# Kernel optimization log

Hardware: AMD Instinct MI355X
Metric: run time of the kernel (lower is better)

Reference implementation:

```python
import jax, jax.numpy as jnp
import numpy as np

H = 8      # num_attention_heads
DH = 96    # attention_head_size
LN_EPS = 1e-5


def setup_inputs() -> dict:
    key = jax.random.key(0)
    ks = jax.random.split(key, 12)
    B, S, D = 2, 768, 768
    sc = 0.02
    return {
        "hidden_states": jax.random.normal(ks[0], (B, S, D), jnp.float32),
        "distance_matrix": jax.random.uniform(ks[1], (B, S, S), jnp.float32) * 20.0,
        "angle_matrix": jax.random.uniform(ks[2], (B, S, S), jnp.float32) * np.pi,
        "attention_mask": jnp.ones((B, S), jnp.float32),
        "Wq": jax.random.normal(ks[3], (D, D), jnp.float32) * sc,
        "bq": jnp.zeros((D,), jnp.float32),
        "Wk": jax.random.normal(ks[4], (D, D), jnp.float32) * sc,
        "bk": jnp.zeros((D,), jnp.float32),
        "Wv": jax.random.normal(ks[5], (D, D), jnp.float32) * sc,
        "bv": jnp.zeros((D,), jnp.float32),
        "Wd": jax.random.normal(ks[6], (DH,), jnp.float32) * sc,
        "bd": jnp.zeros((DH,), jnp.float32),
        "Wa": jax.random.normal(ks[7], (DH,), jnp.float32) * sc,
        "ba": jnp.zeros((DH,), jnp.float32),
        "Wo": jax.random.normal(ks[8], (D, D), jnp.float32) * sc,
        "bo": jnp.zeros((D,), jnp.float32),
        "ln_g": jnp.ones((D,), jnp.float32),
        "ln_b": jnp.zeros((D,), jnp.float32),
    }


def _heads(x, B, S):
    # [B,S,D] -> [B,H,S,DH]
    return x.reshape(B, S, H, DH).transpose(0, 2, 1, 3)


def reference(hidden_states, distance_matrix, angle_matrix, attention_mask,
              Wq, bq, Wk, bk, Wv, bv, Wd, bd, Wa, ba, Wo, bo, ln_g, ln_b):
    B, S, D = hidden_states.shape
    q = _heads(hidden_states @ Wq.T + bq, B, S)   # [B,H,S,DH]
    k = _heads(hidden_states @ Wk.T + bk, B, S)
    v = _heads(hidden_states @ Wv.T + bv, B, S)

    scores = jnp.einsum('bhid,bhjd->bhij', q, k) / jnp.sqrt(jnp.float32(DH))

    # distance / angle relative-position biases: emb[b,i,j,:] = dist[b,i,j]*Wd + bd
    dist_emb = distance_matrix[..., None] * Wd + bd   # [B,S,S,DH]
    scores = scores + jnp.einsum('bhid,bijd->bhij', q, dist_emb)
    ang_emb = angle_matrix[..., None] * Wa + ba       # [B,S,S,DH]
    scores = scores + jnp.einsum('bhid,bijd->bhij', q, ang_emb)

    # key mask, broadcast over heads and query positions
    scores = scores + (1.0 - attention_mask)[:, None, None, :] * -10000.0

    probs = jax.nn.softmax(scores, axis=-1)           # [B,H,S,S]
    ctx = jnp.einsum('bhij,bhjd->bhid', probs, v)
    ctx = ctx.transpose(0, 2, 1, 3).reshape(B, S, D)  # [B,S,D]

    out = ctx @ Wo.T + bo
    x = out + hidden_states
    mu = jnp.mean(x, axis=-1, keepdims=True)
    var = jnp.var(x, axis=-1, keepdims=True)
    out = (x - mu) * jax.lax.rsqrt(var + LN_EPS) * ln_g + ln_b
    return out, probs
```

## Files before the change

kernel.cpp:

```cpp
#include <hip/hip_runtime.h>
#include <stdint.h>

#define B_  2
#define S_  768
#define D_  768
#define H_  8
#define DH_ 96

typedef unsigned short ushort_t;
typedef __bf16 bf16x8 __attribute__((ext_vector_type(8)));
typedef float  f32x4  __attribute__((ext_vector_type(4)));

__device__ inline ushort_t f2bf(float f) {
    union { float f; unsigned int u; } v; v.f = f;
    unsigned int u = v.u;
    unsigned int r = u + 0x7fffu + ((u >> 16) & 1u);
    return (ushort_t)(r >> 16);
}
__device__ inline float bf2f(ushort_t u) {
    union { unsigned int i; float f; } c; c.i = ((unsigned int)u) << 16;
    return c.f;
}

__device__ inline void glds16(const void* gp, void* lp) {
    auto g = reinterpret_cast<const __attribute__((address_space(1))) uint32_t*>(
        reinterpret_cast<uintptr_t>(gp));
    auto l = reinterpret_cast<__attribute__((address_space(3))) uint32_t*>(
        reinterpret_cast<uintptr_t>(lp));
    __builtin_amdgcn_global_load_lds(g, l, 16, 0, 0);
}

__global__ __launch_bounds__(256) void k_convert(
        const float* __restrict__ X, const float* __restrict__ Wq,
        const float* __restrict__ Wk, const float* __restrict__ Wv,
        const float* __restrict__ Wo,
        ushort_t* __restrict__ Xb, ushort_t* __restrict__ Wb) {
    const int NX4 = (B_ * S_ * D_) / 4;
    const int NW4 = (D_ * D_) / 4;
    int i = blockIdx.x * blockDim.x + threadIdx.x;
    float4 v;
    ushort_t* dst;
    if (i < NX4) {
        v = ((const float4*)X)[i];
        dst = Xb + i * 4;
    } else {
        int wi = i - NX4;
        int sel = wi / NW4;
        int off = wi - sel * NW4;
        const float* src = (sel == 0) ? Wq : (sel == 1) ? Wk : (sel == 2) ? Wv : Wo;
        v = ((const float4*)src)[off];
        dst = Wb + wi * 4;
    }
    ushort4 o;
    o.x = f2bf(v.x); o.y = f2bf(v.y); o.z = f2bf(v.z); o.w = f2bf(v.w);
    *(ushort4*)dst = o;
}

__device__ inline void gemm64_glds(
        const ushort_t* __restrict__ A, int lda,
        const ushort_t* __restrict__ Bt, int ldb,
        int K, int m0, int n0,
        ushort_t* As, ushort_t* Bs, f32x4 acc[2][2]) {
    const int tid  = threadIdx.x;
    const int lane = tid & 63, wave = tid >> 6;
    const int wm = (wave >> 1) * 32, wn = (wave & 1) * 32;
    const int fr = lane & 15, fk = (lane >> 4) * 8;
    const int sr = wave * 16 + (lane >> 2);
    const int sc = (lane & 3) * 8;
    const ushort_t* Ap = A  + (size_t)(m0 + sr) * lda + sc;
    const ushort_t* Bp = Bt + (size_t)(n0 + sr) * ldb + sc;
    ushort_t* AsW = As + wave * 512;
    ushort_t* BsW = Bs + wave * 512;
    for (int kt = 0; kt < K; kt += 32) {
        if (kt) __syncthreads();
        glds16(Ap + kt, AsW);
        glds16(Bp + kt, BsW);
        __syncthreads();
        bf16x8 a0 = *(const bf16x8*)&As[(wm      + fr) * 32 + fk];
        bf16x8 a1 = *(const bf16x8*)&As[(wm + 16 + fr) * 32 + fk];
        bf16x8 b0 = *(const bf16x8*)&Bs[(wn      + fr) * 32 + fk];
        bf16x8 b1 = *(const bf16x8*)&Bs[(wn + 16 + fr) * 32 + fk];
        acc[0][0] = __builtin_amdgcn_mfma_f32_16x16x32_bf16(a0, b0, acc[0][0], 0, 0, 0);
        acc[0][1] = __builtin_amdgcn_mfma_f32_16x16x32_bf16(a0, b1, acc[0][1], 0, 0, 0);
        acc[1][0] = __builtin_amdgcn_mfma_f32_16x16x32_bf16(a1, b0, acc[1][0], 0, 0, 0);
        acc[1][1] = __builtin_amdgcn_mfma_f32_16x16x32_bf16(a1, b1, acc[1][1], 0, 0, 0);
    }
}

__global__ __launch_bounds__(256) void k_qkv(
        const ushort_t* __restrict__ Xb, const ushort_t* __restrict__ Wb,
        const float* __restrict__ bq, const float* __restrict__ bk,
        const float* __restrict__ bv,
        ushort_t* __restrict__ Qb, ushort_t* __restrict__ Kb,
        ushort_t* __restrict__ Vtb) {
    __shared__ __align__(16) ushort_t As[64 * 32];
    __shared__ __align__(16) ushort_t Bs[64 * 32];
    f32x4 acc[2][2];
    #pragma unroll
    for (int i = 0; i < 2; i++)
        #pragma unroll
        for (int j = 0; j < 2; j++) acc[i][j] = (f32x4){0.f, 0.f, 0.f, 0.f};
    const int m0 = blockIdx.y * 64, n0 = blockIdx.x * 64;
    gemm64_glds(Xb, D_, Wb, D_, D_, m0, n0, As, Bs, acc);
    const int lane = threadIdx.x & 63, wave = threadIdx.x >> 6;
    const int wm = (wave >> 1) * 32, wn = (wave & 1) * 32;
    #pragma unroll
    for (int ni = 0; ni < 2; ni++) {
        int gcol = n0 + wn + ni * 16 + (lane & 15);
        int g = gcol / D_, d768 = gcol - g * D_;
        int h = d768 / DH_, d = d768 - h * DH_;
        float bias = (g == 0 ? bq : (g == 1 ? bk : bv))[d768];
        #pragma unroll
        for (int mi = 0; mi < 2; mi++) {
            #pragma unroll
            for (int r = 0; r < 4; r++) {
                int grow = m0 + wm + mi * 16 + (lane >> 4) * 4 + r;
                int b = grow / S_, s = grow - b * S_;
                ushort_t ob = f2bf(acc[mi][ni][r] + bias);
                int bh = b * H_ + h;
                if (g == 0)      Qb[((size_t)bh * S_ + s) * DH_ + d] = ob;
                else if (g == 1) Kb[((size_t)bh * S_ + s) * DH_ + d] = ob;
                else             Vtb[((size_t)bh * DH_ + d) * S_ + s] = ob;
            }
        }
    }
}

__global__ __launch_bounds__(256) void k_qcoef(
        const ushort_t* __restrict__ Qb,
        const float* __restrict__ Wd, const float* __restrict__ bd,
        const float* __restrict__ Wa, const float* __restrict__ ba,
        float* __restrict__ qcoef) {
    const int wave = threadIdx.x >> 6, lane = threadIdx.x & 63;
    const int row = blockIdx.x * 4 + wave;
    const ushort_t* q = Qb + (size_t)row * DH_;
    float e0 = bf2f(q[lane]);
    float c0 = e0 * Wd[lane];
    float c1 = e0 * Wa[lane];
    float c2 = e0 * (bd[lane] + ba[lane]);
    if (lane < 32) {
        int d = 64 + lane;
        float e1 = bf2f(q[d]);
        c0 += e1 * Wd[d];
        c1 += e1 * Wa[d];
        c2 += e1 * (bd[d] + ba[d]);
    }
    #pragma unroll
    for (int o = 32; o > 0; o >>= 1) {
        c0 += __shfl_down(c0, o);
        c1 += __shfl_down(c1, o);
        c2 += __shfl_down(c2, o);
    }
    if (lane == 0) {
        qcoef[row * 3 + 0] = c0;
        qcoef[row * 3 + 1] = c1;
        qcoef[row * 3 + 2] = c2;
    }
}

#define L1B 29696
__global__ __launch_bounds__(256) void k_flash(
        const ushort_t* __restrict__ Qb, const ushort_t* __restrict__ Kb,
        const ushort_t* __restrict__ Vtb, const float* __restrict__ qcoef,
        const float* __restrict__ distm, const float* __restrict__ angm,
        const float* __restrict__ mask,
        float* __restrict__ probs, ushort_t* __restrict__ Ctxb) {
    __shared__ __align__(16) char sm[2 * L1B + 640];
    float* mstat = (float*)(sm + 2 * L1B);
    float* lstat = (float*)(sm + 2 * L1B + 256);
    float* linv  = (float*)(sm + 2 * L1B + 512);
    const int idx = blockIdx.x;
    const int h = idx / 48, rem = idx - h * 48;
    const int b = rem / 24, r0 = (rem - b * 24) * 32;
    const int bh = b * H_ + h;
    const int tid = threadIdx.x, lane = tid & 63, w = tid >> 6;
    const int frn = lane & 15, fko = (lane >> 4) * 8, frg4 = (lane >> 4) * 4;
    const int rg = w & 1, cp = w >> 1;
    const ushort_t* Qbh = Qb + (size_t)bh * S_ * DH_;
    const ushort_t* Kbh = Kb + (size_t)bh * S_ * DH_;
    const ushort_t* Vbh = Vtb + (size_t)bh * DH_ * S_;

    bf16x8 aq[3];
    {
        const ushort_t* qp = Qbh + (size_t)(r0 + rg * 16 + frn) * DH_ + fko;
        aq[0] = *(const bf16x8*)qp;
        aq[1] = *(const bf16x8*)(qp + 32);
        aq[2] = *(const bf16x8*)(qp + 64);
    }
    float qc0[4], qc1[4], qc2[4];
    #pragma unroll
    for (int r = 0; r < 4; r++) {
        const float* qp = qcoef + ((size_t)bh * S_ + r0 + rg * 16 + frg4 + r) * 3;
        qc0[r] = qp[0]; qc1[r] = qp[1]; qc2[r] = qp[2];
    }
    const float isq = 0.10206207261596577f;

    f32x4 acc[24];
    #pragma unroll
    for (int c = 0; c < 12; ++c) {
        char* bufc = sm + (c & 1) * L1B;
        ushort_t* Ks = (ushort_t*)bufc;
        float* Dd = (float*)(bufc + 12288);
        float* Da = (float*)(bufc + 20992);
        #pragma unroll
        for (int k = 0; k < 3; ++k) {
            int i = tid + 256 * k;
            int row = i / 12, cc = (i - row * 12) * 8;
            *(uint4*)(Ks + row * 96 + cc) =
                *(const uint4*)(Kbh + (size_t)(c * 64 + row) * DH_ + cc);
        }
        #pragma unroll
        for (int k = 0; k < 2; ++k) {
            int i = tid + 256 * k;
            int row = i >> 4, c4 = (i & 15) * 4;
            size_t src = ((size_t)b * S_ + r0 + row) * S_ + c * 64 + c4;
            *(float4*)(Dd + row * 68 + c4) = *(const float4*)(distm + src);
            *(float4*)(Da + row * 68 + c4) = *(const float4*)(angm + src);
        }
        __syncthreads();
        #pragma unroll
        for (int tt = 0; tt < 2; ++tt) {
            const ushort_t* kp = Ks + (cp * 32 + tt * 16 + frn) * 96 + fko;
            f32x4 ca = (f32x4){0.f, 0.f, 0.f, 0.f};
            ca = __builtin_amdgcn_mfma_f32_16x16x32_bf16(aq[0], *(const bf16x8*)kp, ca, 0, 0, 0);
            ca = __builtin_amdgcn_mfma_f32_16x16x32_bf16(aq[1], *(const bf16x8*)(kp + 32), ca, 0, 0, 0);
            ca = __builtin_amdgcn_mfma_f32_16x16x32_bf16(aq[2], *(const bf16x8*)(kp + 64), ca, 0, 0, 0);
            int jl = cp * 32 + tt * 16 + frn;
            float mb = (1.0f - mask[b * S_ + c * 64 + jl]) * -10000.0f;
            #pragma unroll
            for (int r = 0; r < 4; ++r) {
                int rl = rg * 16 + frg4 + r;
                acc[c * 2 + tt][r] = ca[r] * isq + Dd[rl * 68 + jl] * qc0[r]
                                   + Da[rl * 68 + jl] * qc1[r] + qc2[r] + mb;
            }
        }
    }
    float mx[4] = {-1e30f, -1e30f, -1e30f, -1e30f};
    #pragma unroll
    for (int t = 0; t < 24; t++)
        #pragma unroll
        for (int r = 0; r < 4; r++) mx[r] = fmaxf(mx[r], acc[t][r]);
    #pragma unroll
    for (int o = 1; o < 16; o <<= 1)
        #pragma unroll
        for (int r = 0; r < 4; r++) mx[r] = fmaxf(mx[r], __shfl_xor(mx[r], o));
    if (frn == 0)
        #pragma unroll
        for (int r = 0; r < 4; r++) mstat[cp * 32 + rg * 16 + frg4 + r] = mx[r];
    __syncthreads();
    float mf[4], sum[4] = {0.f, 0.f, 0.f, 0.f};
    #pragma unroll
    for (int r = 0; r < 4; r++) {
        int rl = rg * 16 + frg4 + r;
        mf[r] = fmaxf(mstat[rl], mstat[32 + rl]);
    }
    #pragma unroll
    for (int t = 0; t < 24; t++)
        #pragma unroll
        for (int r = 0; r < 4; r++) {
            float e = __expf(acc[t][r] - mf[r]);
            acc[t][r] = e;
            sum[r] += e;
        }
    #pragma unroll
    for (int o = 1; o < 16; o <<= 1)
        #pragma unroll
        for (int r = 0; r < 4; r++) sum[r] += __shfl_xor(sum[r], o);
    if (frn == 0)
        #pragma unroll
        for (int r = 0; r < 4; r++) lstat[cp * 32 + rg * 16 + frg4 + r] = sum[r];
    __syncthreads();
    float inv[4];
    #pragma unroll
    for (int r = 0; r < 4; r++) {
        int rl = rg * 16 + frg4 + r;
        inv[r] = 1.0f / (lstat[rl] + lstat[32 + rl]);
        if (cp == 0 && frn == 0) linv[rl] = inv[r];
    }
    __syncthreads();
    f32x4 accO[3];
    #pragma unroll
    for (int i = 0; i < 3; i++) accO[i] = (f32x4){0.f, 0.f, 0.f, 0.f};
    const int prow = tid >> 3, pc8 = (tid & 7) * 4;
    float* pout = probs + ((size_t)bh * S_ + r0 + prow) * S_;
    const int vrow = tid >> 2, vcv = (tid & 3) * 8;
    const int vrow2 = (tid + 256) >> 2, vcv2 = ((tid + 256) & 3) * 8;
    #pragma unroll
    for (int s = 0; s < 24; ++s) {
        ushort_t* Vs = (ushort_t*)(sm + (s & 1) * 7680);
        ushort_t* Ps = (ushort_t*)(sm + 15360 + (s & 1) * 2560);
        *(uint4*)(Vs + vrow * 40 + vcv) =
            *(const uint4*)(Vbh + (size_t)vrow * S_ + s * 32 + vcv);
        if (tid + 256 < 384)
            *(uint4*)(Vs + vrow2 * 40 + vcv2) =
                *(const uint4*)(Vbh + (size_t)vrow2 * S_ + s * 32 + vcv2);
        if (cp == (s & 1)) {
            #pragma unroll
            for (int tt = 0; tt < 2; ++tt)
                #pragma unroll
                for (int r = 0; r < 4; ++r)
                    Ps[(rg * 16 + frg4 + r) * 40 + tt * 16 + frn] =
                        f2bf(acc[(s & ~1) + tt][r]);
        }
        __syncthreads();
        {
            float iv = linv[prow];
            float4 p4;
            p4.x = bf2f(Ps[prow * 40 + pc8 + 0]) * iv;
            p4.y = bf2f(Ps[prow * 40 + pc8 + 1]) * iv;
            p4.z = bf2f(Ps[prow * 40 + pc8 + 2]) * iv;
            p4.w = bf2f(Ps[prow * 40 + pc8 + 3]) * iv;
            *(float4*)(pout + s * 32 + pc8) = p4;
        }
        bf16x8 a = *(const bf16x8*)&Ps[(rg * 16 + frn) * 40 + fko];
        #pragma unroll
        for (int nt = 0; nt < 3; ++nt) {
            bf16x8 v = *(const bf16x8*)&Vs[(cp * 48 + nt * 16 + frn) * 40 + fko];
            accO[nt] = __builtin_amdgcn_mfma_f32_16x16x32_bf16(a, v, accO[nt], 0, 0, 0);
        }
    }
    #pragma unroll
    for (int nt = 0; nt < 3; ++nt) {
        int col = h * DH_ + cp * 48 + nt * 16 + frn;
        #pragma unroll
        for (int r = 0; r < 4; ++r) {
            int row = r0 + rg * 16 + frg4 + r;
            Ctxb[((size_t)(b * S_ + row)) * D_ + col] = f2bf(accO[nt][r] * inv[r]);
        }
    }
}

__global__ __launch_bounds__(256) void k_out(
        const ushort_t* __restrict__ Ctxb, const ushort_t* __restrict__ Wob,
        const float* __restrict__ bo, const float* __restrict__ hidden,
        float* __restrict__ xbuf) {
    __shared__ __align__(16) ushort_t As[64 * 32];
    __shared__ __align__(16) ushort_t Bs[64 * 32];
    f32x4 acc[2][2];
    #pragma unroll
    for (int i = 0; i < 2; i++)
        #pragma unroll
        for (int j = 0; j < 2; j++) acc[i][j] = (f32x4){0.f, 0.f, 0.f, 0.f};
    const int m0 = blockIdx.y * 64, n0 = blockIdx.x * 64;
    gemm64_glds(Ctxb, D_, Wob, D_, D_, m0, n0, As, Bs, acc);
    const int lane = threadIdx.x & 63, wave = threadIdx.x >> 6;
    const int wm = (wave >> 1) * 32, wn = (wave & 1) * 32;
    #pragma unroll
    for (int ni = 0; ni < 2; ni++) {
        int gcol = n0 + wn + ni * 16 + (lane & 15);
        float bias = bo[gcol];
        #pragma unroll
        for (int mi = 0; mi < 2; mi++) {
            #pragma unroll
            for (int r = 0; r < 4; r++) {
                int grow = m0 + wm + mi * 16 + (lane >> 4) * 4 + r;
                xbuf[(size_t)grow * D_ + gcol] =
                    acc[mi][ni][r] + bias + hidden[(size_t)grow * D_ + gcol];
            }
        }
    }
}

__global__ __launch_bounds__(256) void k_ln(
        const float* __restrict__ xbuf, const float* __restrict__ g,
        const float* __restrict__ bb, float* __restrict__ out) {
    const float* x = xbuf + (size_t)blockIdx.x * D_;
    const int t = threadIdx.x;
    float a0 = x[t], a1 = x[t + 256], a2 = x[t + 512];
    float s = a0 + a1 + a2;
    float ss = a0 * a0 + a1 * a1 + a2 * a2;
    __shared__ float r1[4], r2[4];
    #pragma unroll
    for (int o = 32; o > 0; o >>= 1) { s += __shfl_down(s, o); ss += __shfl_down(ss, o); }
    if ((t & 63) == 0) { r1[t >> 6] = s; r2[t >> 6] = ss; }
    __syncthreads();
    float ts = r1[0] + r1[1] + r1[2] + r1[3];
    float tss = r2[0] + r2[1] + r2[2] + r2[3];
    float mu = ts * (1.0f / D_);
    float var = tss * (1.0f / D_) - mu * mu;
    float rstd = rsqrtf(var + 1e-5f);
    float* o = out + (size_t)blockIdx.x * D_;
    o[t]       = (a0 - mu) * rstd * g[t]       + bb[t];
    o[t + 256] = (a1 - mu) * rstd * g[t + 256] + bb[t + 256];
    o[t + 512] = (a2 - mu) * rstd * g[t + 512] + bb[t + 512];
}

extern "C" void kernel_launch(void* const* d_in, const int* in_sizes, int n_in,
                              void* d_out, int out_size, void* d_ws, size_t ws_size,
                              hipStream_t stream) {
    const float* X     = (const float*)d_in[0];
    const float* distm = (const float*)d_in[1];
    const float* angm  = (const float*)d_in[2];
    const float* mask  = (const float*)d_in[3];
    const float* Wq    = (const float*)d_in[4];
    const float* bq    = (const float*)d_in[5];
    const float* Wk    = (const float*)d_in[6];
    const float* bk    = (const float*)d_in[7];
    const float* Wv    = (const float*)d_in[8];
    const float* bv    = (const float*)d_in[9];
    const float* Wd    = (const float*)d_in[10];
    const float* bd    = (const float*)d_in[11];
    const float* Wa    = (const float*)d_in[12];
    const float* ba    = (const float*)d_in[13];
    const float* Wo    = (const float*)d_in[14];
    const float* bo    = (const float*)d_in[15];
    const float* ln_g  = (const float*)d_in[16];
    const float* ln_b  = (const float*)d_in[17];

    float* outp  = (float*)d_out;
    float* probs = (float*)d_out + (size_t)B_ * S_ * D_;

    char* ws = (char*)d_ws;
    ushort_t* Xb    = (ushort_t*)(ws + 0);
    ushort_t* Wb    = (ushort_t*)(ws + 2359296);
    ushort_t* Qb    = (ushort_t*)(ws + 7077888);
    ushort_t* Kb    = (ushort_t*)(ws + 9437184);
    ushort_t* Vtb   = (ushort_t*)(ws + 11796480);
    ushort_t* Ctxb  = (ushort_t*)(ws + 14155776);
    float*    qcoef = (float*)   (ws + 16515072);
    float*    xbuf  = (float*)   (ws + 16662528);

    k_convert<<<3456, 256, 0, stream>>>(X, Wq, Wk, Wv, Wo, Xb, Wb);
    k_qkv<<<dim3(36, 24), 256, 0, stream>>>(Xb, Wb, bq, bk, bv, Qb, Kb, Vtb);
    k_qcoef<<<3072, 256, 0, stream>>>(Qb, Wd, bd, Wa, ba, qcoef);
    k_flash<<<384, 256, 0, stream>>>(Qb, Kb, Vtb, qcoef, distm, angm, mask, probs, Ctxb);
    k_out<<<dim3(12, 24), 256, 0, stream>>>(Ctxb, Wb + (size_t)2304 * 768, bo, X, xbuf);
    k_ln<<<1536, 256, 0, stream>>>(xbuf, ln_g, ln_b, outp);
}
```

Measured before the change: 180.8 us.

## Enlarge GEMM tiles, fuse qcoef into flash kernel, shrink score chunks

The QKV GEMM moves to 128x128 tiles with a 4x4 MFMA grid per wave, and the output GEMM to 128x64 tiles, so each tile reuses more data but fewer blocks are launched. The separate qcoef kernel is removed: each flash block now computes its query coefficients and the mask bias into shared memory, saving a launch and a global round trip. The score phase walks 32-column chunks with padded LDS strides instead of 64-column ones, which halves shared memory and may reduce bank conflicts. The cost is fewer GEMM blocks (216 and 144) on a large GPU, and more barriers in the flash loop.

Result: slower. 232.8 us (+28.7%).

```diff
diff --git a/kernel.cpp b/kernel.cpp
--- a/kernel.cpp
+++ b/kernel.cpp
@@ -56,68 +56,64 @@
     *(ushort4*)dst = o;
 }
 
-__device__ inline void gemm64_glds(
-        const ushort_t* __restrict__ A, int lda,
-        const ushort_t* __restrict__ Bt, int ldb,
-        int K, int m0, int n0,
-        ushort_t* As, ushort_t* Bs, f32x4 acc[2][2]) {
-    const int tid  = threadIdx.x;
-    const int lane = tid & 63, wave = tid >> 6;
-    const int wm = (wave >> 1) * 32, wn = (wave & 1) * 32;
-    const int fr = lane & 15, fk = (lane >> 4) * 8;
-    const int sr = wave * 16 + (lane >> 2);
-    const int sc = (lane & 3) * 8;
-    const ushort_t* Ap = A  + (size_t)(m0 + sr) * lda + sc;
-    const ushort_t* Bp = Bt + (size_t)(n0 + sr) * ldb + sc;
-    ushort_t* AsW = As + wave * 512;
-    ushort_t* BsW = Bs + wave * 512;
-    for (int kt = 0; kt < K; kt += 32) {
-        if (kt) __syncthreads();
-        glds16(Ap + kt, AsW);
-        glds16(Bp + kt, BsW);
-        __syncthreads();
-        bf16x8 a0 = *(const bf16x8*)&As[(wm      + fr) * 32 + fk];
-        bf16x8 a1 = *(const bf16x8*)&As[(wm + 16 + fr) * 32 + fk];
-        bf16x8 b0 = *(const bf16x8*)&Bs[(wn      + fr) * 32 + fk];
-        bf16x8 b1 = *(const bf16x8*)&Bs[(wn + 16 + fr) * 32 + fk];
-        acc[0][0] = __builtin_amdgcn_mfma_f32_16x16x32_bf16(a0, b0, acc[0][0], 0, 0, 0);
-        acc[0][1] = __builtin_amdgcn_mfma_f32_16x16x32_bf16(a0, b1, acc[0][1], 0, 0, 0);
-        acc[1][0] = __builtin_amdgcn_mfma_f32_16x16x32_bf16(a1, b0, acc[1][0], 0, 0, 0);
-        acc[1][1] = __builtin_amdgcn_mfma_f32_16x16x32_bf16(a1, b1, acc[1][1], 0, 0, 0);
-    }
-}
-
 __global__ __launch_bounds__(256) void k_qkv(
         const ushort_t* __restrict__ Xb, const ushort_t* __restrict__ Wb,
         const float* __restrict__ bq, const float* __restrict__ bk,
         const float* __restrict__ bv,
         ushort_t* __restrict__ Qb, ushort_t* __restrict__ Kb,
         ushort_t* __restrict__ Vtb) {
-    __shared__ __align__(16) ushort_t As[64 * 32];
-    __shared__ __align__(16) ushort_t Bs[64 * 32];
-    f32x4 acc[2][2];
-    #pragma unroll
-    for (int i = 0; i < 2; i++)
-        #pragma unroll
-        for (int j = 0; j < 2; j++) acc[i][j] = (f32x4){0.f, 0.f, 0.f, 0.f};
-    const int m0 = blockIdx.y * 64, n0 = blockIdx.x * 64;
-    gemm64_glds(Xb, D_, Wb, D_, D_, m0, n0, As, Bs, acc);
-    const int lane = threadIdx.x & 63, wave = threadIdx.x >> 6;
-    const int wm = (wave >> 1) * 32, wn = (wave & 1) * 32;
-    #pragma unroll
-    for (int ni = 0; ni < 2; ni++) {
-        int gcol = n0 + wn + ni * 16 + (lane & 15);
-        int g = gcol / D_, d768 = gcol - g * D_;
+    __shared__ __align__(16) ushort_t As[128 * 32];
+    __shared__ __align__(16) ushort_t Bs[128 * 32];
+    const int tid = threadIdx.x, lane = tid & 63, w = tid >> 6;
+    const int frn = lane & 15, fko = (lane >> 4) * 8, frg4 = (lane >> 4) * 4;
+    const int wm = (w & 1) * 64, wn = (w >> 1) * 64;
+    const int m0 = blockIdx.y * 128, n0 = blockIdx.x * 128;
+    const int sr = w * 32 + (lane >> 2), sc = (lane & 3) * 8;
+    const ushort_t* Ap = Xb + (size_t)(m0 + sr) * D_ + sc;
+    const ushort_t* Bp = Wb + (size_t)(n0 + sr) * D_ + sc;
+    ushort_t* AsW = As + w * 1024;
+    ushort_t* BsW = Bs + w * 1024;
+    f32x4 acc[4][4];
+    #pragma unroll
+    for (int i = 0; i < 4; i++)
+        #pragma unroll
+        for (int j = 0; j < 4; j++) acc[i][j] = (f32x4){0.f, 0.f, 0.f, 0.f};
+    for (int kt = 0; kt < D_; kt += 32) {
+        if (kt) __syncthreads();
+        glds16(Ap + kt, AsW);
+        glds16(Ap + 16 * D_ + kt, AsW + 512);
+        glds16(Bp + kt, BsW);
+        glds16(Bp + 16 * D_ + kt, BsW + 512);
+        __syncthreads();
+        bf16x8 a[4], b[4];
+        #pragma unroll
+        for (int mi = 0; mi < 4; mi++)
+            a[mi] = *(const bf16x8*)&As[(wm + mi * 16 + frn) * 32 + fko];
+        #pragma unroll
+        for (int ni = 0; ni < 4; ni++)
+            b[ni] = *(const bf16x8*)&Bs[(wn + ni * 16 + frn) * 32 + fko];
+        #pragma unroll
+        for (int mi = 0; mi < 4; mi++)
+            #pragma unroll
+            for (int ni = 0; ni < 4; ni++)
+                acc[mi][ni] = __builtin_amdgcn_mfma_f32_16x16x32_bf16(a[mi], b[ni], acc[mi][ni], 0, 0, 0);
+    }
+    const int g = n0 / D_;
+    const float* bias_p = (g == 0) ? bq : (g == 1) ? bk : bv;
+    #pragma unroll
+    for (int ni = 0; ni < 4; ni++) {
+        int gcol = n0 + wn + ni * 16 + frn;
+        int d768 = gcol - g * D_;
         int h = d768 / DH_, d = d768 - h * DH_;
-        float bias = (g == 0 ? bq : (g == 1 ? bk : bv))[d768];
-        #pragma unroll
-        for (int mi = 0; mi < 2; mi++) {
+        float bias = bias_p[d768];
+        #pragma unroll
+        for (int mi = 0; mi < 4; mi++) {
             #pragma unroll
             for (int r = 0; r < 4; r++) {
-                int grow = m0 + wm + mi * 16 + (lane >> 4) * 4 + r;
-                int b = grow / S_, s = grow - b * S_;
+                int grow = m0 + wm + mi * 16 + frg4 + r;
+                int bidx = grow / S_, s = grow - bidx * S_;
                 ushort_t ob = f2bf(acc[mi][ni][r] + bias);
-                int bh = b * H_ + h;
+                int bh = bidx * H_ + h;
                 if (g == 0)      Qb[((size_t)bh * S_ + s) * DH_ + d] = ob;
                 else if (g == 1) Kb[((size_t)bh * S_ + s) * DH_ + d] = ob;
                 else             Vtb[((size_t)bh * DH_ + d) * S_ + s] = ob;
@@ -126,49 +122,23 @@
     }
 }
 
-__global__ __launch_bounds__(256) void k_qcoef(
-        const ushort_t* __restrict__ Qb,
+#define KSLD 104
+#define DLD  36
+#define L1B  15872
+__global__ __launch_bounds__(256) void k_flash(
+        const ushort_t* __restrict__ Qb, const ushort_t* __restrict__ Kb,
+        const ushort_t* __restrict__ Vtb,
         const float* __restrict__ Wd, const float* __restrict__ bd,
         const float* __restrict__ Wa, const float* __restrict__ ba,
-        float* __restrict__ qcoef) {
-    const int wave = threadIdx.x >> 6, lane = threadIdx.x & 63;
-    const int row = blockIdx.x * 4 + wave;
-    const ushort_t* q = Qb + (size_t)row * DH_;
-    float e0 = bf2f(q[lane]);
-    float c0 = e0 * Wd[lane];
-    float c1 = e0 * Wa[lane];
-    float c2 = e0 * (bd[lane] + ba[lane]);
-    if (lane < 32) {
-        int d = 64 + lane;
-        float e1 = bf2f(q[d]);
-        c0 += e1 * Wd[d];
-        c1 += e1 * Wa[d];
-        c2 += e1 * (bd[d] + ba[d]);
-    }
-    #pragma unroll
-    for (int o = 32; o > 0; o >>= 1) {
-        c0 += __shfl_down(c0, o);
-        c1 += __shfl_down(c1, o);
-        c2 += __shfl_down(c2, o);
-    }
-    if (lane == 0) {
-        qcoef[row * 3 + 0] = c0;
-        qcoef[row * 3 + 1] = c1;
-        qcoef[row * 3 + 2] = c2;
-    }
-}
-
-#define L1B 29696
-__global__ __launch_bounds__(256) void k_flash(
-        const ushort_t* __restrict__ Qb, const ushort_t* __restrict__ Kb,
-        const ushort_t* __restrict__ Vtb, const float* __restrict__ qcoef,
         const float* __restrict__ distm, const float* __restrict__ angm,
         const float* __restrict__ mask,
         float* __restrict__ probs, ushort_t* __restrict__ Ctxb) {
-    __shared__ __align__(16) char sm[2 * L1B + 640];
-    float* mstat = (float*)(sm + 2 * L1B);
-    float* lstat = (float*)(sm + 2 * L1B + 256);
-    float* linv  = (float*)(sm + 2 * L1B + 512);
+    __shared__ __align__(16) char sm[35840];
+    float* mstat = (float*)(sm + 31744);
+    float* lstat = (float*)(sm + 32000);
+    float* linv  = (float*)(sm + 32256);
+    float* Ms    = (float*)(sm + 32384);
+    float* qcS   = (float*)(sm + 35456);
     const int idx = blockIdx.x;
     const int h = idx / 48, rem = idx - h * 48;
     const int b = rem / 24, r0 = (rem - b * 24) * 32;
@@ -180,6 +150,30 @@
     const ushort_t* Kbh = Kb + (size_t)bh * S_ * DH_;
     const ushort_t* Vbh = Vtb + (size_t)bh * DH_ * S_;
 
+    Ms[tid]       = (1.0f - mask[b * S_ + tid])       * -10000.0f;
+    Ms[tid + 256] = (1.0f - mask[b * S_ + tid + 256]) * -10000.0f;
+    Ms[tid + 512] = (1.0f - mask[b * S_ + tid + 512]) * -10000.0f;
+
+    {
+        const int qr = tid >> 3, p = tid & 7;
+        const ushort_t* qrow = Qbh + (size_t)(r0 + qr) * DH_;
+        float c0 = 0.f, c1 = 0.f, c2 = 0.f;
+        #pragma unroll
+        for (int j = 0; j < 12; j++) {
+            int d = p * 12 + j;
+            float e = bf2f(qrow[d]);
+            c0 += e * Wd[d];
+            c1 += e * Wa[d];
+            c2 += e * (bd[d] + ba[d]);
+        }
+        #pragma unroll
+        for (int o = 1; o < 8; o <<= 1) {
+            c0 += __shfl_xor(c0, o);
+            c1 += __shfl_xor(c1, o);
+            c2 += __shfl_xor(c2, o);
+        }
+        if (p == 0) { qcS[qr * 3] = c0; qcS[qr * 3 + 1] = c1; qcS[qr * 3 + 2] = c2; }
+    }
     bf16x8 aq[3];
     {
         const ushort_t* qp = Qbh + (size_t)(r0 + rg * 16 + frn) * DH_ + fko;
@@ -187,54 +181,50 @@
         aq[1] = *(const bf16x8*)(qp + 32);
         aq[2] = *(const bf16x8*)(qp + 64);
     }
+    __syncthreads();
     float qc0[4], qc1[4], qc2[4];
     #pragma unroll
     for (int r = 0; r < 4; r++) {
-        const float* qp = qcoef + ((size_t)bh * S_ + r0 + rg * 16 + frg4 + r) * 3;
-        qc0[r] = qp[0]; qc1[r] = qp[1]; qc2[r] = qp[2];
+        int rl = rg * 16 + frg4 + r;
+        qc0[r] = qcS[rl * 3]; qc1[r] = qcS[rl * 3 + 1]; qc2[r] = qcS[rl * 3 + 2];
     }
     const float isq = 0.10206207261596577f;
 
+    const int kr0r = tid / 12,         kc0 = (tid - kr0r * 12) * 8;
+    const int kr1r = (tid + 256) / 12, kc1 = ((tid + 256) % 12) * 8;
+    const int drow = tid >> 3, dc4 = (tid & 7) * 4;
+
     f32x4 acc[24];
     #pragma unroll
-    for (int c = 0; c < 12; ++c) {
+    for (int c = 0; c < 24; ++c) {
         char* bufc = sm + (c & 1) * L1B;
         ushort_t* Ks = (ushort_t*)bufc;
-        float* Dd = (float*)(bufc + 12288);
-        float* Da = (float*)(bufc + 20992);
-        #pragma unroll
-        for (int k = 0; k < 3; ++k) {
-            int i = tid + 256 * k;
-            int row = i / 12, cc = (i - row * 12) * 8;
-            *(uint4*)(Ks + row * 96 + cc) =
-                *(const uint4*)(Kbh + (size_t)(c * 64 + row) * DH_ + cc);
-        }
-        #pragma unroll
-        for (int k = 0; k < 2; ++k) {
-            int i = tid + 256 * k;
-            int row = i >> 4, c4 = (i & 15) * 4;
-            size_t src = ((size_t)b * S_ + r0 + row) * S_ + c * 64 + c4;
-            *(float4*)(Dd + row * 68 + c4) = *(const float4*)(distm + src);
-            *(float4*)(Da + row * 68 + c4) = *(const float4*)(angm + src);
-        }
+        float* Dd = (float*)(bufc + 6656);
+        float* Da = (float*)(bufc + 11264);
+        *(uint4*)(Ks + kr0r * KSLD + kc0) =
+            *(const uint4*)(Kbh + (size_t)(c * 32 + kr0r) * DH_ + kc0);
+        if (tid < 128)
+            *(uint4*)(Ks + kr1r * KSLD + kc1) =
+                *(const uint4*)(Kbh + (size_t)(c * 32 + kr1r) * DH_ + kc1);
+        size_t ds = ((size_t)b * S_ + r0 + drow) * S_ + c * 32 + dc4;
+        *(float4*)(Dd + drow * DLD + dc4) = *(const float4*)(distm + ds);
+        *(float4*)(Da + drow * DLD + dc4) = *(const float4*)(angm + ds);
         __syncthreads();
-        #pragma unroll
-        for (int tt = 0; tt < 2; ++tt) {
-            const ushort_t* kp = Ks + (cp * 32 + tt * 16 + frn) * 96 + fko;
-            f32x4 ca = (f32x4){0.f, 0.f, 0.f, 0.f};
-            ca = __builtin_amdgcn_mfma_f32_16x16x32_bf16(aq[0], *(const bf16x8*)kp, ca, 0, 0, 0);
-            ca = __builtin_amdgcn_mfma_f32_16x16x32_bf16(aq[1], *(const bf16x8*)(kp + 32), ca, 0, 0, 0);
-            ca = __builtin_amdgcn_mfma_f32_16x16x32_bf16(aq[2], *(const bf16x8*)(kp + 64), ca, 0, 0, 0);
-            int jl = cp * 32 + tt * 16 + frn;
-            float mb = (1.0f - mask[b * S_ + c * 64 + jl]) * -10000.0f;
-            #pragma unroll
-            for (int r = 0; r < 4; ++r) {
-                int rl = rg * 16 + frg4 + r;
-                acc[c * 2 + tt][r] = ca[r] * isq + Dd[rl * 68 + jl] * qc0[r]
-                                   + Da[rl * 68 + jl] * qc1[r] + qc2[r] + mb;
-            }
-        }
-    }
+        const ushort_t* kp = Ks + (cp * 16 + frn) * KSLD + fko;
+        f32x4 ca = (f32x4){0.f, 0.f, 0.f, 0.f};
+        ca = __builtin_amdgcn_mfma_f32_16x16x32_bf16(aq[0], *(const bf16x8*)kp, ca, 0, 0, 0);
+        ca = __builtin_amdgcn_mfma_f32_16x16x32_bf16(aq[1], *(const bf16x8*)(kp + 32), ca, 0, 0, 0);
+        ca = __builtin_amdgcn_mfma_f32_16x16x32_bf16(aq[2], *(const bf16x8*)(kp + 64), ca, 0, 0, 0);
+        const int jl = cp * 16 + frn;
+        float mb = Ms[c * 32 + jl];
+        #pragma unroll
+        for (int r = 0; r < 4; ++r) {
+            int rl = rg * 16 + frg4 + r;
+            acc[c][r] = ca[r] * isq + Dd[rl * DLD + jl] * qc0[r]
+                      + Da[rl * DLD + jl] * qc1[r] + qc2[r] + mb;
+        }
+    }
+
     float mx[4] = {-1e30f, -1e30f, -1e30f, -1e30f};
     #pragma unroll
     for (int t = 0; t < 24; t++)
@@ -278,6 +268,7 @@
         if (cp == 0 && frn == 0) linv[rl] = inv[r];
     }
     __syncthreads();
+
     f32x4 accO[3];
     #pragma unroll
     for (int i = 0; i < 3; i++) accO[i] = (f32x4){0.f, 0.f, 0.f, 0.f};
@@ -285,23 +276,19 @@
     float* pout = probs + ((size_t)bh * S_ + r0 + prow) * S_;
     const int vrow = tid >> 2, vcv = (tid & 3) * 8;
     const int vrow2 = (tid + 256) >> 2, vcv2 = ((tid + 256) & 3) * 8;
+    const bool hasv2 = (tid < 128);
     #pragma unroll
     for (int s = 0; s < 24; ++s) {
         ushort_t* Vs = (ushort_t*)(sm + (s & 1) * 7680);
         ushort_t* Ps = (ushort_t*)(sm + 15360 + (s & 1) * 2560);
         *(uint4*)(Vs + vrow * 40 + vcv) =
             *(const uint4*)(Vbh + (size_t)vrow * S_ + s * 32 + vcv);
-        if (tid + 256 < 384)
+        if (hasv2)
             *(uint4*)(Vs + vrow2 * 40 + vcv2) =
                 *(const uint4*)(Vbh + (size_t)vrow2 * S_ + s * 32 + vcv2);
-        if (cp == (s & 1)) {
-            #pragma unroll
-            for (int tt = 0; tt < 2; ++tt)
-                #pragma unroll
-                for (int r = 0; r < 4; ++r)
-                    Ps[(rg * 16 + frg4 + r) * 40 + tt * 16 + frn] =
-                        f2bf(acc[(s & ~1) + tt][r]);
-        }
+        #pragma unroll
+        for (int r = 0; r < 4; ++r)
+            Ps[(rg * 16 + frg4 + r) * 40 + cp * 16 + frn] = f2bf(acc[s][r]);
         __syncthreads();
         {
             float iv = linv[prow];
@@ -334,26 +321,51 @@
         const ushort_t* __restrict__ Ctxb, const ushort_t* __restrict__ Wob,
         const float* __restrict__ bo, const float* __restrict__ hidden,
         float* __restrict__ xbuf) {
-    __shared__ __align__(16) ushort_t As[64 * 32];
+    __shared__ __align__(16) ushort_t As[128 * 32];
     __shared__ __align__(16) ushort_t Bs[64 * 32];
-    f32x4 acc[2][2];
-    #pragma unroll
-    for (int i = 0; i < 2; i++)
+    const int tid = threadIdx.x, lane = tid & 63, w = tid >> 6;
+    const int frn = lane & 15, fko = (lane >> 4) * 8, frg4 = (lane >> 4) * 4;
+    const int wm = (w & 1) * 64, wn = (w >> 1) * 32;
+    const int m0 = blockIdx.y * 128, n0 = blockIdx.x * 64;
+    const int sr = w * 32 + (lane >> 2), sc = (lane & 3) * 8;
+    const int srB = w * 16 + (lane >> 2);
+    const ushort_t* Ap = Ctxb + (size_t)(m0 + sr) * D_ + sc;
+    const ushort_t* Bp = Wob + (size_t)(n0 + srB) * D_ + sc;
+    ushort_t* AsW = As + w * 1024;
+    ushort_t* BsW = Bs + w * 512;
+    f32x4 acc[4][2];
+    #pragma unroll
+    for (int i = 0; i < 4; i++)
         #pragma unroll
         for (int j = 0; j < 2; j++) acc[i][j] = (f32x4){0.f, 0.f, 0.f, 0.f};
-    const int m0 = blockIdx.y * 64, n0 = blockIdx.x * 64;
-    gemm64_glds(Ctxb, D_, Wob, D_, D_, m0, n0, As, Bs, acc);
-    const int lane = threadIdx.x & 63, wave = threadIdx.x >> 6;
-    const int wm = (wave >> 1) * 32, wn = (wave & 1) * 32;
+    for (int kt = 0; kt < D_; kt += 32) {
+        if (kt) __syncthreads();
+        glds16(Ap + kt, AsW);
+        glds16(Ap + 16 * D_ + kt, AsW + 512);
+        glds16(Bp + kt, BsW);
+        __syncthreads();
+        bf16x8 a[4], b[2];
+        #pragma unroll
+        for (int mi = 0; mi < 4; mi++)
+            a[mi] = *(const bf16x8*)&As[(wm + mi * 16 + frn) * 32 + fko];
+        #pragma unroll
+        for (int ni = 0; ni < 2; ni++)
+            b[ni] = *(const bf16x8*)&Bs[(wn + ni * 16 + frn) * 32 + fko];
+        #pragma unroll
+        for (int mi = 0; mi < 4; mi++)
+            #pragma unroll
+            for (int ni = 0; ni < 2; ni++)
+                acc[mi][ni] = __builtin_amdgcn_mfma_f32_16x16x32_bf16(a[mi], b[ni], acc[mi][ni], 0, 0, 0);
+    }
     #pragma unroll
     for (int ni = 0; ni < 2; ni++) {
-        int gcol = n0 + wn + ni * 16 + (lane & 15);
+        int gcol = n0 + wn + ni * 16 + frn;
         float bias = bo[gcol];
         #pragma unroll
-        for (int mi = 0; mi < 2; mi++) {
+        for (int mi = 0; mi < 4; mi++) {
             #pragma unroll
             for (int r = 0; r < 4; r++) {
-                int grow = m0 + wm + mi * 16 + (lane >> 4) * 4 + r;
+                int grow = m0 + wm + mi * 16 + frg4 + r;
                 xbuf[(size_t)grow * D_ + gcol] =
                     acc[mi][ni][r] + bias + hidden[(size_t)grow * D_ + gcol];
             }
@@ -417,13 +429,11 @@
     ushort_t* Kb    = (ushort_t*)(ws + 9437184);
     ushort_t* Vtb   = (ushort_t*)(ws + 11796480);
     ushort_t* Ctxb  = (ushort_t*)(ws + 14155776);
-    float*    qcoef = (float*)   (ws + 16515072);
-    float*    xbuf  = (float*)   (ws + 16662528);
+    float*    xbuf  = (float*)   (ws + 16515072);
 
     k_convert<<<3456, 256, 0, stream>>>(X, Wq, Wk, Wv, Wo, Xb, Wb);
-    k_qkv<<<dim3(36, 24), 256, 0, stream>>>(Xb, Wb, bq, bk, bv, Qb, Kb, Vtb);
-    k_qcoef<<<3072, 256, 0, stream>>>(Qb, Wd, bd, Wa, ba, qcoef);
-    k_flash<<<384, 256, 0, stream>>>(Qb, Kb, Vtb, qcoef, distm, angm, mask, probs, Ctxb);
-    k_out<<<dim3(12, 24), 256, 0, stream>>>(Ctxb, Wb + (size_t)2304 * 768, bo, X, xbuf);
+    k_qkv<<<dim3(18, 12), 256, 0, stream>>>(Xb, Wb, bq, bk, bv, Qb, Kb, Vtb);
+    k_flash<<<384, 256, 0, stream>>>(Qb, Kb, Vtb, Wd, bd, Wa, ba, distm, angm, mask, probs, Ctxb);
+    k_out<<<dim3(12, 12), 256, 0, stream>>>(Ctxb, Wb + (size_t)2304 * 768, bo, X, xbuf);
     k_ln<<<1536, 256, 0, stream>>>(xbuf, ln_g, ln_b, outp);
 }
```
